# Optimization experiments

Measured on AMD Instinct MI355X. Metric: run time of the kernel, lower is better.

Reference implementation:

```python
import jax, jax.numpy as jnp
import numpy as np

NUM_CODES = 8192
DIM = 8
BETA = 0.25
TAU = 1.0
EPS = 1e-10


def setup_inputs() -> dict:
    key = jax.random.key(0)
    k1, k2, k3 = jax.random.split(key, 3)
    z_e = jax.random.normal(k1, (8, DIM, 32, 32), dtype=jnp.float32)
    embedding = jax.random.normal(k2, (NUM_CODES, DIM), dtype=jnp.float32) * 0.01
    proj_w = jax.random.normal(k3, (NUM_CODES, DIM), dtype=jnp.float32) * (1.0 / np.sqrt(DIM))
    return {"z_e": z_e, "embedding": embedding, "proj_w": proj_w}


def reference(z_e, embedding, proj_w):
    B, D, H, W = z_e.shape
    K = embedding.shape[0]
    # (B, D, H, W) -> (N, D), N = B*H*W  (matches permute(0,2,3,1).reshape(-1,d))
    z_flat = jnp.transpose(z_e, (0, 2, 3, 1)).reshape(-1, D)
    # 1x1 conv == matmul against (K, D) weight
    logits = z_flat @ proj_w.T  # (N, K)  -- dominant memory traffic
    # Gumbel-softmax with hard=True (training path), fixed noise key
    u = jax.random.uniform(jax.random.key(42), logits.shape,
                           dtype=logits.dtype, minval=1e-20, maxval=1.0)
    gumbel = -jnp.log(-jnp.log(u))
    y_soft = jax.nn.softmax((logits + gumbel) / TAU, axis=-1)
    idx = jnp.argmax(y_soft, axis=-1)  # (N,)
    y_hard = jax.nn.one_hot(idx, K, dtype=y_soft.dtype)
    # straight-through: forward = hard one-hot, backward = soft
    st = y_hard + y_soft - jax.lax.stop_gradient(y_soft)
    z_q_flat = st @ embedding  # (N, D) -- effectively a gather in forward
    z_q = jnp.transpose(z_q_flat.reshape(B, H, W, D), (0, 3, 1, 2))
    # commitment loss against detached re-lookup
    q_flat = jax.lax.stop_gradient(embedding[idx])
    commit_loss = BETA * jnp.mean((z_flat - q_flat) ** 2)
    # usage stats (no-grad in original)
    counts = jnp.zeros((K,), z_e.dtype).at[idx].add(1.0)
    avg = counts / idx.shape[0]
    perplexity = jnp.exp(-jnp.sum(avg * jnp.log(avg + EPS)))
    usage = jnp.sum(counts > 0).astype(z_e.dtype) / K
    indices = idx.reshape(B, H, W)
    return z_q, indices, commit_loss, perplexity, usage
```

## Files before the change

kernel.cpp:

```cpp
#include <hip/hip_runtime.h>
#include <stdint.h>


#define NCODES 8192
#define NROWS  8192
#define HALF_OFF 33554432u

__device__ __forceinline__ uint32_t gvq16_rotl(uint32_t x, uint32_t r) {
    return (x << r) | (x >> (32u - r));
}

__device__ __forceinline__ void gvq16_threefry(uint32_t& x0, uint32_t& x1) {
    const uint32_t ks0 = 0u, ks1 = 42u, ks2 = 42u ^ 0x1BD11BDAu;
    x0 += ks0; x1 += ks1;
#define TFR(r) { x0 += x1; x1 = gvq16_rotl(x1, r); x1 ^= x0; }
    TFR(13u) TFR(15u) TFR(26u) TFR(6u)   x0 += ks1; x1 += ks2 + 1u;
    TFR(17u) TFR(29u) TFR(16u) TFR(24u)  x0 += ks2; x1 += ks0 + 2u;
    TFR(13u) TFR(15u) TFR(26u) TFR(6u)   x0 += ks0; x1 += ks1 + 3u;
    TFR(17u) TFR(29u) TFR(16u) TFR(24u)  x0 += ks1; x1 += ks2 + 4u;
    TFR(13u) TFR(15u) TFR(26u) TFR(6u)   x0 += ks2; x1 += ks0 + 5u;
#undef TFR
}

#define GVQ_C   0.36651292058166435f
#define GVQ_LN2 0.69314718055994530942f
__device__ __forceinline__ float gvq16_gumbel(uint32_t bits) {
    float u = __uint_as_float((bits >> 9) | 0x3f800000u) - 1.0f;
    float l1 = __builtin_amdgcn_logf(u);
    float l2 = __builtin_amdgcn_logf(0.0f - l1);
    return fmaf(-GVQ_LN2, l2, GVQ_C);
}

__global__ __launch_bounds__(64) void gvq16_init(float* out) {
    if (threadIdx.x == 0) out[73728] = 0.0f;
}

__global__ __launch_bounds__(256, 4) void gvq16_argmax(const float* __restrict__ z_e,
                                                       const float* __restrict__ proj_w,
                                                       const float* __restrict__ emb,
                                                       float* __restrict__ out) {
    __shared__ float sv0[256]; __shared__ int si0[256];
    __shared__ float sv1[256]; __shared__ int si1[256];
    __shared__ float ssq[2];
    const int tid = threadIdx.x;
    const int n0 = blockIdx.x;
    const int n1 = n0 + 4096;
    const int b0 = n0 >> 10, r0 = n0 & 1023;
    const int b1 = n1 >> 10, r1 = n1 & 1023;

    float z0[8], z1[8];
#pragma unroll
    for (int d = 0; d < 8; ++d) {
        z0[d] = z_e[b0 * 8192 + d * 1024 + r0];
        z1[d] = z_e[b1 * 8192 + d * 1024 + r1];
    }

    const float4* wr = (const float4*)proj_w;
    float best0 = -INFINITY, best1 = -INFINITY;
    int bi0 = 0, bi1 = 0;
    const uint32_t base0 = (uint32_t)n0 * (uint32_t)NCODES;

    for (int k = tid; k < NCODES; k += 256) {
        float4 wa = wr[2 * k];
        float4 wb = wr[2 * k + 1];

        float d0 = 0.0f, d1 = 0.0f;
        d0 = fmaf(z0[0], wa.x, d0); d1 = fmaf(z1[0], wa.x, d1);
        d0 = fmaf(z0[1], wa.y, d0); d1 = fmaf(z1[1], wa.y, d1);
        d0 = fmaf(z0[2], wa.z, d0); d1 = fmaf(z1[2], wa.z, d1);
        d0 = fmaf(z0[3], wa.w, d0); d1 = fmaf(z1[3], wa.w, d1);
        d0 = fmaf(z0[4], wb.x, d0); d1 = fmaf(z1[4], wb.x, d1);
        d0 = fmaf(z0[5], wb.y, d0); d1 = fmaf(z1[5], wb.y, d1);
        d0 = fmaf(z0[6], wb.z, d0); d1 = fmaf(z1[6], wb.z, d1);
        d0 = fmaf(z0[7], wb.w, d0); d1 = fmaf(z1[7], wb.w, d1);

        uint32_t a0 = 0u, a1 = base0 + (uint32_t)k;
        uint32_t c0 = 0u, c1 = base0 + HALF_OFF + (uint32_t)k;
        gvq16_threefry(a0, a1);
        gvq16_threefry(c0, c1);
        float v0 = d0 + gvq16_gumbel(a0 ^ a1);
        float v1 = d1 + gvq16_gumbel(c0 ^ c1);

        if (v0 > best0) { best0 = v0; bi0 = k; }
        if (v1 > best1) { best1 = v1; bi1 = k; }
    }

    sv0[tid] = best0; si0[tid] = bi0;
    sv1[tid] = best1; si1[tid] = bi1;
    __syncthreads();
    for (int s = 128; s > 0; s >>= 1) {
        if (tid < s) {
            if (sv0[tid + s] > sv0[tid] ||
                (sv0[tid + s] == sv0[tid] && si0[tid + s] < si0[tid])) {
                sv0[tid] = sv0[tid + s]; si0[tid] = si0[tid + s];
            }
            if (sv1[tid + s] > sv1[tid] ||
                (sv1[tid + s] == sv1[tid] && si1[tid + s] < si1[tid])) {
                sv1[tid] = sv1[tid + s]; si1[tid] = si1[tid + s];
            }
        }
        __syncthreads();
    }

    if (tid < 2) {
        const int n = (tid == 0) ? n0 : n1;
        const int idx = (tid == 0) ? si0[0] : si1[0];
        const float* zz = (tid == 0) ? z0 : z1;
        out[65536 + n] = (float)idx;
        const float4* ep = (const float4*)(emb + idx * 8);
        float4 ea = ep[0], eb = ep[1];
        float e[8] = {ea.x, ea.y, ea.z, ea.w, eb.x, eb.y, eb.z, eb.w};
        const int b = n >> 10, r = n & 1023;
        float sq = 0.0f;
#pragma unroll
        for (int d = 0; d < 8; ++d) {
            out[b * 8192 + d * 1024 + r] = e[d];
            float diff = zz[d] - e[d];
            sq = fmaf(diff, diff, sq);
        }
        ssq[tid] = sq;
    }
    __syncthreads();
    if (tid == 0) atomicAdd(out + 73728, ssq[0] + ssq[1]);
}

__global__ __launch_bounds__(1024) void gvq16_stats(float* __restrict__ out) {
    __shared__ int counts[NCODES];
    __shared__ float hred[1024];
    __shared__ int ired[1024];
    const int tid = threadIdx.x;

    for (int k = tid; k < NCODES; k += 1024) counts[k] = 0;
    __syncthreads();

    for (int n = tid; n < NROWS; n += 1024) {
        int idx = (int)out[65536 + n] & 8191;
        atomicAdd(&counts[idx], 1);
    }
    __syncthreads();

    float h = 0.0f; int used = 0;
    for (int k = tid; k < NCODES; k += 1024) {
        int c = counts[k];
        float avg = (float)c * (1.0f / 8192.0f);
        h += avg * logf(avg + 1e-10f);
        used += (c > 0) ? 1 : 0;
    }
    hred[tid] = h; ired[tid] = used;
    __syncthreads();
    for (int t = 512; t > 0; t >>= 1) {
        if (tid < t) { hred[tid] += hred[tid + t]; ired[tid] += ired[tid + t]; }
        __syncthreads();
    }
    if (tid == 0) {
        float accum = out[73728];
        out[73728] = 0.25f * accum * (1.0f / 65536.0f);
        out[73729] = expf(-hred[0]);
        out[73730] = (float)ired[0] * (1.0f / 8192.0f);
    }
}

extern "C" void kernel_launch(void* const* d_in, const int* in_sizes, int n_in,
                              void* d_out, int out_size, void* d_ws, size_t ws_size,
                              hipStream_t stream) {
    const float* z_e   = (const float*)d_in[0];
    const float* emb   = (const float*)d_in[1];
    const float* projw = (const float*)d_in[2];
    float* out = (float*)d_out;

    gvq16_init  <<<1,    64,   0, stream>>>(out);
    gvq16_argmax<<<4096, 256,  0, stream>>>(z_e, projw, emb, out);
    gvq16_stats <<<1,    1024, 0, stream>>>(out);
}
```

Before: 244.9 us.

## Hand-schedule threefry in inline asm, 4 rows per block, global histogram

The Gumbel noise generator is rewritten as interleaved inline-asm Threefry for four rows at once. It uses v_alignbit rotates, v_add3 and constant folding of key-schedule adds, with x0=0 folded away and the counter advanced incrementally. Each block now handles four rows instead of two, so proj_w loads are reused across more rows. The histogram moves into a global device array updated by atomics in the argmax kernel, which removes the shared-memory counting pass from the single-block stats kernel. The main target is the ALU cost of the RNG, at the price of hand-written asm that must exactly reproduce the JAX random bits.

```diff
diff --git a/kernel.cpp b/kernel.cpp
--- a/kernel.cpp
+++ b/kernel.cpp
@@ -4,109 +4,170 @@
 
 #define NCODES 8192
 #define NROWS  8192
-#define HALF_OFF 33554432u
-
-__device__ __forceinline__ uint32_t gvq16_rotl(uint32_t x, uint32_t r) {
-    return (x << r) | (x >> (32u - r));
-}
-
-__device__ __forceinline__ void gvq16_threefry(uint32_t& x0, uint32_t& x1) {
-    const uint32_t ks0 = 0u, ks1 = 42u, ks2 = 42u ^ 0x1BD11BDAu;
-    x0 += ks0; x1 += ks1;
-#define TFR(r) { x0 += x1; x1 = gvq16_rotl(x1, r); x1 ^= x0; }
-    TFR(13u) TFR(15u) TFR(26u) TFR(6u)   x0 += ks1; x1 += ks2 + 1u;
-    TFR(17u) TFR(29u) TFR(16u) TFR(24u)  x0 += ks2; x1 += ks0 + 2u;
-    TFR(13u) TFR(15u) TFR(26u) TFR(6u)   x0 += ks0; x1 += ks1 + 3u;
-    TFR(17u) TFR(29u) TFR(16u) TFR(24u)  x0 += ks1; x1 += ks2 + 4u;
-    TFR(13u) TFR(15u) TFR(26u) TFR(6u)   x0 += ks2; x1 += ks0 + 5u;
-#undef TFR
-}
+
+__device__ int g_hist[NCODES];
+
+
+#define TF4_R1 \
+  "v_mov_b32 %4, %8\n" "v_mov_b32 %5, %9\n" \
+  "v_mov_b32 %6, %10\n" "v_mov_b32 %7, %11\n" \
+  "v_alignbit_b32 %0, %8, %8, 19\n" "v_alignbit_b32 %1, %9, %9, 19\n" \
+  "v_alignbit_b32 %2, %10, %10, 19\n" "v_alignbit_b32 %3, %11, %11, 19\n" \
+  "v_xor_b32 %0, %0, %4\n" "v_xor_b32 %1, %1, %5\n" \
+  "v_xor_b32 %2, %2, %6\n" "v_xor_b32 %3, %3, %7\n"
+
+#define TF4_ADD \
+  "v_add_u32 %4, %4, %0\n" "v_add_u32 %5, %5, %1\n" \
+  "v_add_u32 %6, %6, %2\n" "v_add_u32 %7, %7, %3\n"
+
+#define TF4_ADD3_42 \
+  "v_add3_u32 %4, %4, %0, 42\n" "v_add3_u32 %5, %5, %1, 42\n" \
+  "v_add3_u32 %6, %6, %2, 42\n" "v_add3_u32 %7, %7, %3, 42\n"
+
+#define TF4_ROT(s) \
+  "v_alignbit_b32 %0, %0, %0, " #s "\n" "v_alignbit_b32 %1, %1, %1, " #s "\n" \
+  "v_alignbit_b32 %2, %2, %2, " #s "\n" "v_alignbit_b32 %3, %3, %3, " #s "\n"
+
+#define TF4_XOR \
+  "v_xor_b32 %0, %0, %4\n" "v_xor_b32 %1, %1, %5\n" \
+  "v_xor_b32 %2, %2, %6\n" "v_xor_b32 %3, %3, %7\n"
+
+#define TF4_AX1(lit) \
+  "v_add_u32 %0, " #lit ", %0\n" "v_add_u32 %1, " #lit ", %1\n" \
+  "v_add_u32 %2, " #lit ", %2\n" "v_add_u32 %3, " #lit ", %3\n"
+
+#define TF4_AX0(lit) \
+  "v_add_u32 %4, " #lit ", %4\n" "v_add_u32 %5, " #lit ", %5\n" \
+  "v_add_u32 %6, " #lit ", %6\n" "v_add_u32 %7, " #lit ", %7\n"
+
+#define TF4_RN(s)  TF4_ADD     TF4_ROT(s) TF4_XOR
+#define TF4_RN3(s) TF4_ADD3_42 TF4_ROT(s) TF4_XOR
 
 #define GVQ_C   0.36651292058166435f
 #define GVQ_LN2 0.69314718055994530942f
-__device__ __forceinline__ float gvq16_gumbel(uint32_t bits) {
+__device__ __forceinline__ float gvq17_gumbel(uint32_t bits) {
     float u = __uint_as_float((bits >> 9) | 0x3f800000u) - 1.0f;
     float l1 = __builtin_amdgcn_logf(u);
     float l2 = __builtin_amdgcn_logf(0.0f - l1);
     return fmaf(-GVQ_LN2, l2, GVQ_C);
 }
 
-__global__ __launch_bounds__(64) void gvq16_init(float* out) {
-    if (threadIdx.x == 0) out[73728] = 0.0f;
-}
-
-__global__ __launch_bounds__(256, 4) void gvq16_argmax(const float* __restrict__ z_e,
+__global__ __launch_bounds__(1024) void gvq17_init(float* out) {
+    const int t = threadIdx.x;
+    for (int k = t; k < NCODES; k += 1024) g_hist[k] = 0;
+    if (t == 0) out[73728] = 0.0f;
+}
+
+#define DOT8(zz) \
+    fmaf(zz[7], wb.w, fmaf(zz[6], wb.z, fmaf(zz[5], wb.y, fmaf(zz[4], wb.x, \
+    fmaf(zz[3], wa.w, fmaf(zz[2], wa.z, fmaf(zz[1], wa.y, zz[0] * wa.x)))))))
+
+__global__ __launch_bounds__(256, 5) void gvq17_argmax(const float* __restrict__ z_e,
                                                        const float* __restrict__ proj_w,
                                                        const float* __restrict__ emb,
                                                        float* __restrict__ out) {
-    __shared__ float sv0[256]; __shared__ int si0[256];
-    __shared__ float sv1[256]; __shared__ int si1[256];
-    __shared__ float ssq[2];
+    __shared__ float sv[4][256];
+    __shared__ int   sj[4][256];
+    __shared__ float ssq[4];
     const int tid = threadIdx.x;
-    const int n0 = blockIdx.x;
-    const int n1 = n0 + 4096;
-    const int b0 = n0 >> 10, r0 = n0 & 1023;
-    const int b1 = n1 >> 10, r1 = n1 & 1023;
-
-    float z0[8], z1[8];
+    const int n0 = blockIdx.x * 4;
+
+    float z0[8], z1[8], z2[8], z3[8];
+    {
+        const int b = n0 >> 10, r = n0 & 1023;
+        (void)b; (void)r;
+    }
 #pragma unroll
     for (int d = 0; d < 8; ++d) {
-        z0[d] = z_e[b0 * 8192 + d * 1024 + r0];
-        z1[d] = z_e[b1 * 8192 + d * 1024 + r1];
-    }
-
-    const float4* wr = (const float4*)proj_w;
-    float best0 = -INFINITY, best1 = -INFINITY;
-    int bi0 = 0, bi1 = 0;
-    const uint32_t base0 = (uint32_t)n0 * (uint32_t)NCODES;
-
-    for (int k = tid; k < NCODES; k += 256) {
-        float4 wa = wr[2 * k];
-        float4 wb = wr[2 * k + 1];
-
-        float d0 = 0.0f, d1 = 0.0f;
-        d0 = fmaf(z0[0], wa.x, d0); d1 = fmaf(z1[0], wa.x, d1);
-        d0 = fmaf(z0[1], wa.y, d0); d1 = fmaf(z1[1], wa.y, d1);
-        d0 = fmaf(z0[2], wa.z, d0); d1 = fmaf(z1[2], wa.z, d1);
-        d0 = fmaf(z0[3], wa.w, d0); d1 = fmaf(z1[3], wa.w, d1);
-        d0 = fmaf(z0[4], wb.x, d0); d1 = fmaf(z1[4], wb.x, d1);
-        d0 = fmaf(z0[5], wb.y, d0); d1 = fmaf(z1[5], wb.y, d1);
-        d0 = fmaf(z0[6], wb.z, d0); d1 = fmaf(z1[6], wb.z, d1);
-        d0 = fmaf(z0[7], wb.w, d0); d1 = fmaf(z1[7], wb.w, d1);
-
-        uint32_t a0 = 0u, a1 = base0 + (uint32_t)k;
-        uint32_t c0 = 0u, c1 = base0 + HALF_OFF + (uint32_t)k;
-        gvq16_threefry(a0, a1);
-        gvq16_threefry(c0, c1);
-        float v0 = d0 + gvq16_gumbel(a0 ^ a1);
-        float v1 = d1 + gvq16_gumbel(c0 ^ c1);
+        const int nA = n0 + 0, nB = n0 + 1, nC = n0 + 2, nD = n0 + 3;
+        z0[d] = z_e[(nA >> 10) * 8192 + d * 1024 + (nA & 1023)];
+        z1[d] = z_e[(nB >> 10) * 8192 + d * 1024 + (nB & 1023)];
+        z2[d] = z_e[(nC >> 10) * 8192 + d * 1024 + (nC & 1023)];
+        z3[d] = z_e[(nD >> 10) * 8192 + d * 1024 + (nD & 1023)];
+    }
+
+    uint32_t ca = ((uint32_t)(n0 + 0) << 13) + (uint32_t)tid + 42u;
+    uint32_t cb = ((uint32_t)(n0 + 1) << 13) + (uint32_t)tid + 42u;
+    uint32_t cc = ((uint32_t)(n0 + 2) << 13) + (uint32_t)tid + 42u;
+    uint32_t cd = ((uint32_t)(n0 + 3) << 13) + (uint32_t)tid + 42u;
+
+    const float4* p = ((const float4*)proj_w) + 2 * tid;
+    float best0 = -INFINITY, best1 = -INFINITY, best2 = -INFINITY, best3 = -INFINITY;
+    int bi0 = 0, bi1 = 0, bi2 = 0, bi3 = 0;
+    int k = tid;
+
+    for (int i = 0; i < 32; ++i) {
+        float4 wa = p[0];
+        float4 wb = p[1];
+        p += 512;
+
+        float d0 = DOT8(z0);
+        float d1 = DOT8(z1);
+        float d2 = DOT8(z2);
+        float d3 = DOT8(z3);
+
+        uint32_t o0, o1, o2, o3, t0, t1, t2, t3;
+        asm(TF4_R1
+            TF4_RN(17) TF4_RN(6) TF4_RN(26)
+            TF4_AX1(0x1BD11BF1)
+            TF4_RN3(15) TF4_RN(3) TF4_RN(16) TF4_RN(8)
+            TF4_AX0(0x1BD11BF0) TF4_AX1(2)
+            TF4_RN(19) TF4_RN(17) TF4_RN(6) TF4_RN(26)
+            TF4_AX1(45)
+            TF4_RN(15) TF4_RN(3) TF4_RN(16) TF4_RN(8)
+            TF4_AX1(0x1BD11BF4)
+            TF4_RN3(19) TF4_RN(17) TF4_RN(6) TF4_RN(26)
+            TF4_AX0(0x1BD11BF0) TF4_AX1(5)
+            TF4_XOR
+            : "=&v"(o0), "=&v"(o1), "=&v"(o2), "=&v"(o3),
+              "=&v"(t0), "=&v"(t1), "=&v"(t2), "=&v"(t3)
+            : "v"(ca), "v"(cb), "v"(cc), "v"(cd));
+        (void)t0; (void)t1; (void)t2; (void)t3;
+
+        float v0 = d0 + gvq17_gumbel(o0);
+        float v1 = d1 + gvq17_gumbel(o1);
+        float v2 = d2 + gvq17_gumbel(o2);
+        float v3 = d3 + gvq17_gumbel(o3);
 
         if (v0 > best0) { best0 = v0; bi0 = k; }
         if (v1 > best1) { best1 = v1; bi1 = k; }
-    }
-
-    sv0[tid] = best0; si0[tid] = bi0;
-    sv1[tid] = best1; si1[tid] = bi1;
+        if (v2 > best2) { best2 = v2; bi2 = k; }
+        if (v3 > best3) { best3 = v3; bi3 = k; }
+
+        ca += 256u; cb += 256u; cc += 256u; cd += 256u;
+        k += 256;
+    }
+
+    sv[0][tid] = best0; sj[0][tid] = bi0;
+    sv[1][tid] = best1; sj[1][tid] = bi1;
+    sv[2][tid] = best2; sj[2][tid] = bi2;
+    sv[3][tid] = best3; sj[3][tid] = bi3;
     __syncthreads();
     for (int s = 128; s > 0; s >>= 1) {
         if (tid < s) {
-            if (sv0[tid + s] > sv0[tid] ||
-                (sv0[tid + s] == sv0[tid] && si0[tid + s] < si0[tid])) {
-                sv0[tid] = sv0[tid + s]; si0[tid] = si0[tid + s];
-            }
-            if (sv1[tid + s] > sv1[tid] ||
-                (sv1[tid + s] == sv1[tid] && si1[tid + s] < si1[tid])) {
-                sv1[tid] = sv1[tid + s]; si1[tid] = si1[tid + s];
+#pragma unroll
+            for (int r = 0; r < 4; ++r) {
+                float va = sv[r][tid + s];
+                if (va > sv[r][tid] ||
+                    (va == sv[r][tid] && sj[r][tid + s] < sj[r][tid])) {
+                    sv[r][tid] = va; sj[r][tid] = sj[r][tid + s];
+                }
             }
         }
         __syncthreads();
     }
 
-    if (tid < 2) {
-        const int n = (tid == 0) ? n0 : n1;
-        const int idx = (tid == 0) ? si0[0] : si1[0];
-        const float* zz = (tid == 0) ? z0 : z1;
+    if (tid < 4) {
+        const int n = n0 + tid;
+        const int idx = sj[tid][0];
         out[65536 + n] = (float)idx;
+        atomicAdd(&g_hist[idx], 1);
+        float zz[8];
+#pragma unroll
+        for (int d = 0; d < 8; ++d) {
+            zz[d] = (tid == 0) ? z0[d] : (tid == 1) ? z1[d]
+                  : (tid == 2) ? z2[d] : z3[d];
+        }
         const float4* ep = (const float4*)(emb + idx * 8);
         float4 ea = ep[0], eb = ep[1];
         float e[8] = {ea.x, ea.y, ea.z, ea.w, eb.x, eb.y, eb.z, eb.w};
@@ -121,27 +182,18 @@
         ssq[tid] = sq;
     }
     __syncthreads();
-    if (tid == 0) atomicAdd(out + 73728, ssq[0] + ssq[1]);
-}
-
-__global__ __launch_bounds__(1024) void gvq16_stats(float* __restrict__ out) {
-    __shared__ int counts[NCODES];
+    if (tid == 0)
+        atomicAdd(out + 73728, ssq[0] + ssq[1] + ssq[2] + ssq[3]);
+}
+
+__global__ __launch_bounds__(1024) void gvq17_stats(float* __restrict__ out) {
     __shared__ float hred[1024];
-    __shared__ int ired[1024];
+    __shared__ int   ired[1024];
     const int tid = threadIdx.x;
 
-    for (int k = tid; k < NCODES; k += 1024) counts[k] = 0;
-    __syncthreads();
-
-    for (int n = tid; n < NROWS; n += 1024) {
-        int idx = (int)out[65536 + n] & 8191;
-        atomicAdd(&counts[idx], 1);
-    }
-    __syncthreads();
-
     float h = 0.0f; int used = 0;
-    for (int k = tid; k < NCODES; k += 1024) {
-        int c = counts[k];
+    for (int kk = tid; kk < NCODES; kk += 1024) {
+        int c = g_hist[kk];
         float avg = (float)c * (1.0f / 8192.0f);
         h += avg * logf(avg + 1e-10f);
         used += (c > 0) ? 1 : 0;
@@ -168,7 +220,7 @@
     const float* projw = (const float*)d_in[2];
     float* out = (float*)d_out;
 
-    gvq16_init  <<<1,    64,   0, stream>>>(out);
-    gvq16_argmax<<<4096, 256,  0, stream>>>(z_e, projw, emb, out);
-    gvq16_stats <<<1,    1024, 0, stream>>>(out);
-}
+    gvq17_init  <<<1,    1024, 0, stream>>>(out);
+    gvq17_argmax<<<2048, 256,  0, stream>>>(z_e, projw, emb, out);
+    gvq17_stats <<<1,    1024, 0, stream>>>(out);
+}
```

Measured after the change: 212.4 us. 13.3% less time.
